# Kernel tuning notes

Hardware: AMD Instinct MI355X
Metric: run time of the kernel (lower is better)

Reference implementation:

```python
import jax, jax.numpy as jnp
import numpy as np

N_STREAMS = 4096


def setup_inputs() -> dict:
    key = jax.random.key(0)
    # Plain Gaussian (well-separated singular values; the polar factor math is
    # identical to the module's eye + 0.01*randn init, just a different point).
    H_raw = jax.random.normal(key, (N_STREAMS, N_STREAMS), dtype=jnp.float32)
    return {"H_raw": H_raw}


def reference(H_raw) -> jnp.ndarray:
    # OrthogonalMixing.forward: orthogonal polar factor of H_raw via thin SVD.
    U, s, Vh = jnp.linalg.svd(H_raw, full_matrices=False)
    return U @ Vh  # (s, s), satisfies H^T H = I
```

## Files before the change

### kernel.cpp

```cpp
#include <hip/hip_runtime.h>
#include <hip/hip_bf16.h>
#include <hip/hip_fp16.h>

#define NN 4096
#define NGROW 8
#define NPOL 2
#define NITER (NGROW + NPOL)
#define NPOW 12
#define NKT (NN / 64)
#define NTRI 136
#define PRESCALE 32.0f

using f16 = _Float16;
typedef __attribute__((ext_vector_type(4))) float f32x4;
typedef __attribute__((ext_vector_type(8))) f16 h16x8;

__device__ inline void gl_lds16(const void* g, void* l) {
  __builtin_amdgcn_global_load_lds(
      (const __attribute__((address_space(1))) unsigned int*)(unsigned long long)(uintptr_t)g,
      (__attribute__((address_space(3))) unsigned int*)(uintptr_t)l,
      16, 0, 0);
}

template <int EPI, int TRI>
__global__ __launch_bounds__(512, 2) void gemm_nt(
    const f16* __restrict__ P, const f16* __restrict__ Q,
    void* __restrict__ Out, const f16* __restrict__ aux,
    float alpha, float beta) {
  int bi, bj;
  if (TRI) {
    const int t = blockIdx.x;
    int r = (int)((sqrtf(8.0f * (float)t + 1.0f) - 1.0f) * 0.5f);
    while ((r + 1) * (r + 2) / 2 <= t) ++r;
    while (r * (r + 1) / 2 > t) --r;
    bi = r;
    bj = t - r * (r + 1) / 2;
  } else {
    bi = blockIdx.x;
    bj = blockIdx.y;
  }

  __shared__ f16 lA[2][256 * 64];
  __shared__ f16 lB[2][256 * 64];

  const int tid = threadIdx.x;
  const int lane = tid & 63;
  const int wv = tid >> 6;
  const int wr = wv >> 2;
  const int wc = wv & 3;
  const int m = lane & 15;
  const int qd = lane >> 4;
  const int srow = tid >> 3;
  const int schk = tid & 7;

  f32x4 acc[8][4] = {};
  h16x8 avA[2][2], avB[2][2];
  h16x8 bv0[4][2], bv1[4][2];

#define STAGE_A(u_, kk_, b_)                                                  \
  do {                                                                        \
    const int rr_ = (u_)*64 + srow;                                           \
    gl_lds16(P + (size_t)(bi * 256 + rr_) * NN + (kk_) + ((schk ^ (srow & 7)) * 8), \
             &lA[b_][(u_)*4096 + tid * 8]);                                   \
  } while (0)
#define STAGE_B(u_, kk_, b_)                                                  \
  do {                                                                        \
    const int rr_ = (u_)*64 + srow;                                           \
    gl_lds16(Q + (size_t)(bj * 256 + rr_) * NN + (kk_) + ((schk ^ (srow & 7)) * 8), \
             &lB[b_][(u_)*4096 + tid * 8]);                                   \
  } while (0)

#define READ_AV(dst_, b_, q_)                                                 \
  do {                                                                        \
    _Pragma("unroll") for (int rf = 0; rf < 2; ++rf)                          \
    _Pragma("unroll") for (int ks = 0; ks < 2; ++ks) {                        \
      const int ra = wr * 128 + (q_)*32 + rf * 16 + m;                        \
      const int ca = (ks * 4 + qd) ^ (ra & 7);                                \
      dst_[rf][ks] = *(const h16x8*)&lA[b_][ra * 64 + ca * 8];                \
    }                                                                         \
  } while (0)
#define READ_BV(dst_, b_)                                                     \
  do {                                                                        \
    _Pragma("unroll") for (int cf = 0; cf < 4; ++cf)                          \
    _Pragma("unroll") for (int ks = 0; ks < 2; ++ks) {                        \
      const int rb = wc * 64 + cf * 16 + m;                                   \
      const int cb = (ks * 4 + qd) ^ (rb & 7);                                \
      dst_[cf][ks] = *(const h16x8*)&lB[b_][rb * 64 + cb * 8];                \
    }                                                                         \
  } while (0)
#define MFMA_Q(q_, A_, B_)                                                    \
  do {                                                                        \
    _Pragma("unroll") for (int rf = 0; rf < 2; ++rf)                          \
    _Pragma("unroll") for (int cf = 0; cf < 4; ++cf)                          \
    _Pragma("unroll") for (int ks = 0; ks < 2; ++ks)                          \
        acc[(q_)*2 + rf][cf] = __builtin_amdgcn_mfma_f32_16x16x32_f16(        \
            A_[rf][ks], B_[cf][ks], acc[(q_)*2 + rf][cf], 0, 0, 0);           \
  } while (0)

#define BAR() __builtin_amdgcn_s_barrier()
#define VMCNT(n_) asm volatile("s_waitcnt vmcnt(" #n_ ")" ::: "memory")
#define SGB(m_, n_) __builtin_amdgcn_sched_group_barrier(m_, n_, 0)
#define SGB_RD4_ST2()                                                         \
  do { SGB(0x8,2); SGB(0x100,1); SGB(0x8,2); SGB(0x100,1); SGB(0x8,2);        \
       SGB(0x100,1); SGB(0x8,2); SGB(0x100,1); SGB(0x8,2); SGB(0x30,1);       \
       SGB(0x8,3); SGB(0x30,1); SGB(0x8,3); } while (0)
#define SGB_RD4_ST0()                                                         \
  do { SGB(0x8,3); SGB(0x100,1); SGB(0x8,3); SGB(0x100,1); SGB(0x8,3);        \
       SGB(0x100,1); SGB(0x8,3); SGB(0x100,1); SGB(0x8,4); } while (0)
#define SGB_RD12_ST2()                                                        \
  do { SGB(0x100,2); SGB(0x8,2); SGB(0x100,2); SGB(0x8,2); SGB(0x100,2);      \
       SGB(0x8,2); SGB(0x100,2); SGB(0x8,2); SGB(0x100,2); SGB(0x8,2);        \
       SGB(0x100,2); SGB(0x8,2); SGB(0x30,1); SGB(0x8,2); SGB(0x30,1);        \
       SGB(0x8,2); } while (0)
#define SGB_RD12_ST0()                                                        \
  do { SGB(0x100,2); SGB(0x8,2); SGB(0x100,2); SGB(0x8,2); SGB(0x100,2);      \
       SGB(0x8,2); SGB(0x100,2); SGB(0x8,2); SGB(0x100,2); SGB(0x8,2);        \
       SGB(0x100,2); SGB(0x8,2); SGB(0x8,4); } while (0)

#define TILE_STEADY(t_, b_, nb_, BVC_, BVN_)                                  \
  {                                                                           \
    const int k1 = ((t_) + 1) * 64, k2 = ((t_) + 2) * 64;                     \
                                                                      \
    READ_AV(avB, b_, 1);                                                      \
    STAGE_A(1, k1, nb_); STAGE_A(3, k1, nb_);                                 \
    MFMA_Q(0, avA, BVC_);                                                     \
    SGB_RD4_ST2(); BAR();                                                     \
                                                                      \
    READ_AV(avA, b_, 2);                                                      \
    STAGE_B(0, k2, b_); STAGE_B(1, k2, b_);                                   \
    MFMA_Q(1, avB, BVC_);                                                     \
    SGB_RD4_ST2(); BAR();                                                     \
                                                                      \
    READ_AV(avB, b_, 3);                                                      \
    STAGE_B(2, k2, b_); STAGE_B(3, k2, b_);                                   \
    MFMA_Q(2, avA, BVC_);                                                     \
    SGB_RD4_ST2(); VMCNT(4); BAR();                                           \
                 \
    READ_BV(BVN_, nb_);                                                       \
    READ_AV(avA, nb_, 0);                                                     \
    STAGE_A(0, k2, b_); STAGE_A(2, k2, b_);                                   \
    MFMA_Q(3, avB, BVC_);                                                     \
    SGB_RD12_ST2(); BAR();                                                    \
  }

  STAGE_B(0, 0, 0); STAGE_B(1, 0, 0); STAGE_B(2, 0, 0); STAGE_B(3, 0, 0);
  STAGE_A(0, 0, 0); STAGE_A(1, 0, 0); STAGE_A(2, 0, 0); STAGE_A(3, 0, 0);
  STAGE_B(0, 64, 1); STAGE_B(1, 64, 1); STAGE_B(2, 64, 1); STAGE_B(3, 64, 1);
  STAGE_A(0, 64, 1); STAGE_A(2, 64, 1);
  VMCNT(6);
  BAR();
  READ_BV(bv0, 0);
  READ_AV(avA, 0, 0);
  BAR();

  for (int tt = 0; tt < NKT - 2; tt += 2) {
    TILE_STEADY(tt, 0, 1, bv0, bv1);
    TILE_STEADY(tt + 1, 1, 0, bv1, bv0);
  }

  {
    READ_AV(avB, 0, 1);
    STAGE_A(1, (NKT - 1) * 64, 1); STAGE_A(3, (NKT - 1) * 64, 1);
    MFMA_Q(0, avA, bv0);
    SGB_RD4_ST2(); BAR();
    READ_AV(avA, 0, 2);
    MFMA_Q(1, avB, bv0);
    SGB_RD4_ST0(); BAR();
    READ_AV(avB, 0, 3);
    MFMA_Q(2, avA, bv0);
    SGB_RD4_ST0(); VMCNT(0); BAR();
    READ_BV(bv1, 1);
    READ_AV(avA, 1, 0);
    MFMA_Q(3, avB, bv0);
    SGB_RD12_ST0(); BAR();
  }
  {
    READ_AV(avB, 1, 1);
    MFMA_Q(0, avA, bv1);
    SGB_RD4_ST0(); BAR();
    READ_AV(avA, 1, 2);
    MFMA_Q(1, avB, bv1);
    SGB_RD4_ST0(); BAR();
    READ_AV(avB, 1, 3);
    MFMA_Q(2, avA, bv1);
    SGB_RD4_ST0(); BAR();
    MFMA_Q(3, avB, bv1);
  }

#pragma unroll
  for (int fr = 0; fr < 8; ++fr) {
#pragma unroll
    for (int fc = 0; fc < 4; ++fc) {
#pragma unroll
      for (int rg = 0; rg < 4; ++rg) {
        const int lr = wr * 128 + fr * 16 + qd * 4 + rg;
        const int lc = wc * 64 + fc * 16 + m;
        const size_t idx = (size_t)(bi * 256 + lr) * NN + bj * 256 + lc;
        float v = beta * acc[fr][fc][rg];
        if (alpha != 0.0f) v += alpha * (float)aux[idx];
        if (EPI == 0)
          ((f16*)Out)[idx] = (f16)v;
        else
          ((float*)Out)[idx] = v;
        if (TRI && bi != bj) {
          const size_t idxT = (size_t)(bj * 256 + lc) * NN + bi * 256 + lr;
          ((f16*)Out)[idxT] = (f16)v;
        }
      }
    }
  }
#undef STAGE_A
#undef STAGE_B
#undef READ_AV
#undef READ_BV
#undef MFMA_Q
#undef TILE_STEADY
#undef BAR
#undef VMCNT
#undef SGB
#undef SGB_RD4_ST2
#undef SGB_RD4_ST0
#undef SGB_RD12_ST2
#undef SGB_RD12_ST0
}

__global__ void transpose_h(const unsigned short* __restrict__ in,
                            unsigned short* __restrict__ out) {
  __shared__ unsigned short tile[64][65];
  const int tx = threadIdx.x & 63;
  const int ty = threadIdx.x >> 6;
  const int bx = blockIdx.x, by = blockIdx.y;
#pragma unroll
  for (int rr = 0; rr < 16; ++rr) {
    const int row = rr * 4 + ty;
    tile[row][tx] = in[(size_t)(by * 64 + row) * NN + bx * 64 + tx];
  }
  __syncthreads();
#pragma unroll
  for (int rr = 0; rr < 16; ++rr) {
    const int row = rr * 4 + ty;
    out[(size_t)(bx * 64 + row) * NN + by * 64 + tx] = tile[tx][row];
  }
}

__global__ __launch_bounds__(256) void powmv(const f16* __restrict__ A,
                                             const float* __restrict__ vin,
                                             const float* __restrict__ snin,
                                             float* __restrict__ vout,
                                             float* __restrict__ snout) {
  const float scale = rsqrtf(*snin);
  const int row = blockIdx.x * 4 + (threadIdx.x >> 6);
  const int lane = threadIdx.x & 63;
  const f16* arow = A + (size_t)row * NN;
  float acc = 0.0f;
#pragma unroll
  for (int p = 0; p < 8; ++p) {
    const int c = p * 512 + lane * 8;
    const h16x8 av = *(const h16x8*)(arow + c);
    const float4 w0 = *(const float4*)(vin + c);
    const float4 w1 = *(const float4*)(vin + c + 4);
    acc += (float)av[0] * w0.x + (float)av[1] * w0.y + (float)av[2] * w0.z +
           (float)av[3] * w0.w + (float)av[4] * w1.x + (float)av[5] * w1.y +
           (float)av[6] * w1.z + (float)av[7] * w1.w;
  }
  for (int off = 32; off; off >>= 1) acc += __shfl_down(acc, off, 64);
  if (lane == 0) {
    const float u = acc * scale;
    vout[row] = u;
    atomicAdd(snout, u * u);
  }
}

__global__ void init_pw(float* __restrict__ v0, float* __restrict__ slots) {
  const int t = threadIdx.x;
  if (t < 64) slots[t] = (t == 1) ? 1.0f : 0.0f;
  for (int i = t; i < NN; i += 256) {
    const unsigned h = (unsigned)i * 2654435761u;
    v0[i] = ((h >> 16) & 1) ? 0.015625f : -0.015625f;
  }
}

__global__ void reduce_sumsq(const float* __restrict__ h, float* __restrict__ slots) {
  float acc = 0.0f;
  const size_t total = (size_t)NN * NN;
  for (size_t i = (size_t)blockIdx.x * blockDim.x + threadIdx.x; i < total;
       i += (size_t)gridDim.x * blockDim.x) {
    const float v = h[i];
    acc += v * v;
  }
  for (int off = 32; off; off >>= 1) acc += __shfl_down(acc, off, 64);
  __shared__ float ws[4];
  const int lane = threadIdx.x & 63, wv = threadIdx.x >> 6;
  if (lane == 0) ws[wv] = acc;
  __syncthreads();
  if (threadIdx.x == 0) atomicAdd(&slots[0], ws[0] + ws[1] + ws[2] + ws[3]);
}

__global__ void scale_cast(const float* __restrict__ h, const float* __restrict__ slots,
                           f16* __restrict__ xb, int mode) {
  float inv = rsqrtf(slots[0]) * PRESCALE;
  if (mode) inv *= rsqrtf(1.10f * sqrtf(slots[1 + NPOW]));
  const size_t i = ((size_t)blockIdx.x * blockDim.x + threadIdx.x) * 4;
  const float4 v = *(const float4*)(h + i);
  union { f16 hh[4]; ushort4 u; } cvt;
  cvt.hh[0] = (f16)(v.x * inv);
  cvt.hh[1] = (f16)(v.y * inv);
  cvt.hh[2] = (f16)(v.z * inv);
  cvt.hh[3] = (f16)(v.w * inv);
  *(ushort4*)(xb + i) = cvt.u;
}

__global__ void rescale_f16(f16* __restrict__ a, const float* __restrict__ slots) {
  const float cA = 1.0f / (1.10f * sqrtf(slots[1 + NPOW]));
  const size_t i = ((size_t)blockIdx.x * 256 + threadIdx.x) * 8;
  h16x8 v = *(h16x8*)(a + i);
  h16x8 o;
#pragma unroll
  for (int j = 0; j < 8; ++j) o[j] = (f16)((float)v[j] * cA);
  *(h16x8*)(a + i) = o;
}

extern "C" void kernel_launch(void* const* d_in, const int* in_sizes, int n_in,
                              void* d_out, int out_size, void* d_ws, size_t ws_size,
                              hipStream_t stream) {
  (void)in_sizes; (void)n_in; (void)out_size; (void)ws_size;
  const float* H = (const float*)d_in[0];
  float* out = (float*)d_out;
  char* ws = (char*)d_ws;

  f16* P0 = (f16*)ws;
  f16* P1 = (f16*)(ws + ((size_t)32 << 20));
  f16* Ab = (f16*)(ws + ((size_t)64 << 20));
  f16* Bb = (f16*)((char*)d_out + ((size_t)32 << 20));
  float* v0 = (float*)d_out;
  float* v1 = (float*)((char*)d_out + 16384);
  float* slots = (float*)((char*)d_out + 32768);

  const dim3 gfull(16, 16), tbg(512), tb(256), gt(64, 64);

  init_pw<<<1, 256, 0, stream>>>(v0, slots);
  reduce_sumsq<<<1024, 256, 0, stream>>>(H, slots);
  scale_cast<<<(NN * (size_t)NN) / 4 / 256, 256, 0, stream>>>(H, slots, P0, 0);
  transpose_h<<<gt, tb, 0, stream>>>((const unsigned short*)P0, (unsigned short*)P1);
  gemm_nt<0, 1><<<NTRI, tbg, 0, stream>>>(P1, P1, Ab, (f16*)nullptr, 0.0f, 1.0f);
  for (int k = 0; k < NPOW; ++k) {
    const float* vi = (k & 1) ? v1 : v0;
    float* vo = (k & 1) ? v0 : v1;
    powmv<<<1024, 256, 0, stream>>>(Ab, vi, &slots[1 + k], vo, &slots[2 + k]);
  }
  rescale_f16<<<(NN * (size_t)NN) / 8 / 256, 256, 0, stream>>>(Ab, slots);
  scale_cast<<<(NN * (size_t)NN) / 4 / 256, 256, 0, stream>>>(H, slots, P0, 1);

  f16* X = P0;
  f16* Y = P1;
  const float GA = 3.4445f, GB = -4.7750f, GC = 2.0315f;
  const float PA = 1.875f, PB = -1.25f, PC = 0.375f;

  for (int it = 0; it < NITER; ++it) {
    const bool polish = it >= NGROW;
    const bool last = (it == NITER - 1);
    const float qa = polish ? PA : GA, qb = polish ? PB : GB, qc = polish ? PC : GC;

    if (it > 0) {
      transpose_h<<<gt, tb, 0, stream>>>((const unsigned short*)X, (unsigned short*)Y);
      gemm_nt<0, 1><<<NTRI, tbg, 0, stream>>>(Y, Y, Ab, (f16*)nullptr, 0.0f, 1.0f);
    }
    f16* Bdst = last ? Y : Bb;
    gemm_nt<0, 1><<<NTRI, tbg, 0, stream>>>(Ab, Ab, Bdst, Ab, qb, qc);
    if (!last) {
      gemm_nt<0, 0><<<gfull, tbg, 0, stream>>>(X, Bdst, Y, X, qa, 1.0f);
      f16* t = X; X = Y; Y = t;
    } else {
      gemm_nt<1, 0><<<gfull, tbg, 0, stream>>>(X, Bdst, out, X, qa, 1.0f);
    }
  }
}
```

Before: 4.454 ms.

## Swizzle GEMM block order across XCDs and replace sched barriers with setprio

Block indices are remapped so consecutive hardware block IDs, which are dealt round-robin across the 8 XCDs, map to contiguous tile regions per XCD. This is meant to improve L2 reuse of A/B panels. The full grid becomes 1D (256 blocks). The hand-tuned sched_group_barrier interleaving of LDS reads, stores and MFMAs is removed in favour of raising wave priority around the MFMA clusters. That leaves instruction interleaving to the compiler and may lose the memory/compute overlap the explicit schedule provided.

After: 6.731 ms. +51.1%, slower.

```diff
diff --git a/kernel.cpp b/kernel.cpp
--- a/kernel.cpp
+++ b/kernel.cpp
@@ -29,15 +29,18 @@
     float alpha, float beta) {
   int bi, bj;
   if (TRI) {
-    const int t = blockIdx.x;
+    const int t0 = blockIdx.x;
+    const int t = (t0 & 7) * 17 + (t0 >> 3);
     int r = (int)((sqrtf(8.0f * (float)t + 1.0f) - 1.0f) * 0.5f);
     while ((r + 1) * (r + 2) / 2 <= t) ++r;
     while (r * (r + 1) / 2 > t) --r;
     bi = r;
     bj = t - r * (r + 1) / 2;
   } else {
-    bi = blockIdx.x;
-    bj = blockIdx.y;
+    const int b0 = blockIdx.x;
+    const int sw = (b0 & 7) * 32 + (b0 >> 3);
+    bi = sw >> 4;
+    bj = sw & 15;
   }
 
   __shared__ f16 lA[2][256 * 64];
@@ -98,24 +101,8 @@
   } while (0)
 
 #define BAR() __builtin_amdgcn_s_barrier()
+#define PRIO(x_) __builtin_amdgcn_s_setprio(x_)
 #define VMCNT(n_) asm volatile("s_waitcnt vmcnt(" #n_ ")" ::: "memory")
-#define SGB(m_, n_) __builtin_amdgcn_sched_group_barrier(m_, n_, 0)
-#define SGB_RD4_ST2()                                                         \
-  do { SGB(0x8,2); SGB(0x100,1); SGB(0x8,2); SGB(0x100,1); SGB(0x8,2);        \
-       SGB(0x100,1); SGB(0x8,2); SGB(0x100,1); SGB(0x8,2); SGB(0x30,1);       \
-       SGB(0x8,3); SGB(0x30,1); SGB(0x8,3); } while (0)
-#define SGB_RD4_ST0()                                                         \
-  do { SGB(0x8,3); SGB(0x100,1); SGB(0x8,3); SGB(0x100,1); SGB(0x8,3);        \
-       SGB(0x100,1); SGB(0x8,3); SGB(0x100,1); SGB(0x8,4); } while (0)
-#define SGB_RD12_ST2()                                                        \
-  do { SGB(0x100,2); SGB(0x8,2); SGB(0x100,2); SGB(0x8,2); SGB(0x100,2);      \
-       SGB(0x8,2); SGB(0x100,2); SGB(0x8,2); SGB(0x100,2); SGB(0x8,2);        \
-       SGB(0x100,2); SGB(0x8,2); SGB(0x30,1); SGB(0x8,2); SGB(0x30,1);        \
-       SGB(0x8,2); } while (0)
-#define SGB_RD12_ST0()                                                        \
-  do { SGB(0x100,2); SGB(0x8,2); SGB(0x100,2); SGB(0x8,2); SGB(0x100,2);      \
-       SGB(0x8,2); SGB(0x100,2); SGB(0x8,2); SGB(0x100,2); SGB(0x8,2);        \
-       SGB(0x100,2); SGB(0x8,2); SGB(0x8,4); } while (0)
 
 #define TILE_STEADY(t_, b_, nb_, BVC_, BVN_)                                  \
   {                                                                           \
@@ -123,24 +110,24 @@
                                                                       \
     READ_AV(avB, b_, 1);                                                      \
     STAGE_A(1, k1, nb_); STAGE_A(3, k1, nb_);                                 \
-    MFMA_Q(0, avA, BVC_);                                                     \
-    SGB_RD4_ST2(); BAR();                                                     \
+    PRIO(1); MFMA_Q(0, avA, BVC_); PRIO(0);                                   \
+    BAR();                                                                    \
                                                                       \
     READ_AV(avA, b_, 2);                                                      \
     STAGE_B(0, k2, b_); STAGE_B(1, k2, b_);                                   \
-    MFMA_Q(1, avB, BVC_);                                                     \
-    SGB_RD4_ST2(); BAR();                                                     \
+    PRIO(1); MFMA_Q(1, avB, BVC_); PRIO(0);                                   \
+    BAR();                                                                    \
                                                                       \
     READ_AV(avB, b_, 3);                                                      \
     STAGE_B(2, k2, b_); STAGE_B(3, k2, b_);                                   \
-    MFMA_Q(2, avA, BVC_);                                                     \
-    SGB_RD4_ST2(); VMCNT(4); BAR();                                           \
+    PRIO(1); MFMA_Q(2, avA, BVC_); PRIO(0);                                   \
+    VMCNT(4); BAR();                                                          \
                  \
     READ_BV(BVN_, nb_);                                                       \
     READ_AV(avA, nb_, 0);                                                     \
     STAGE_A(0, k2, b_); STAGE_A(2, k2, b_);                                   \
-    MFMA_Q(3, avB, BVC_);                                                     \
-    SGB_RD12_ST2(); BAR();                                                    \
+    PRIO(1); MFMA_Q(3, avB, BVC_); PRIO(0);                                   \
+    BAR();                                                                    \
   }
 
   STAGE_B(0, 0, 0); STAGE_B(1, 0, 0); STAGE_B(2, 0, 0); STAGE_B(3, 0, 0);
@@ -161,30 +148,30 @@
   {
     READ_AV(avB, 0, 1);
     STAGE_A(1, (NKT - 1) * 64, 1); STAGE_A(3, (NKT - 1) * 64, 1);
-    MFMA_Q(0, avA, bv0);
-    SGB_RD4_ST2(); BAR();
+    PRIO(1); MFMA_Q(0, avA, bv0); PRIO(0);
+    BAR();
     READ_AV(avA, 0, 2);
-    MFMA_Q(1, avB, bv0);
-    SGB_RD4_ST0(); BAR();
+    PRIO(1); MFMA_Q(1, avB, bv0); PRIO(0);
+    BAR();
     READ_AV(avB, 0, 3);
-    MFMA_Q(2, avA, bv0);
-    SGB_RD4_ST0(); VMCNT(0); BAR();
+    PRIO(1); MFMA_Q(2, avA, bv0); PRIO(0);
+    VMCNT(0); BAR();
     READ_BV(bv1, 1);
     READ_AV(avA, 1, 0);
-    MFMA_Q(3, avB, bv0);
-    SGB_RD12_ST0(); BAR();
+    PRIO(1); MFMA_Q(3, avB, bv0); PRIO(0);
+    BAR();
   }
   {
     READ_AV(avB, 1, 1);
-    MFMA_Q(0, avA, bv1);
-    SGB_RD4_ST0(); BAR();
+    PRIO(1); MFMA_Q(0, avA, bv1); PRIO(0);
+    BAR();
     READ_AV(avA, 1, 2);
-    MFMA_Q(1, avB, bv1);
-    SGB_RD4_ST0(); BAR();
+    PRIO(1); MFMA_Q(1, avB, bv1); PRIO(0);
+    BAR();
     READ_AV(avB, 1, 3);
-    MFMA_Q(2, avA, bv1);
-    SGB_RD4_ST0(); BAR();
-    MFMA_Q(3, avB, bv1);
+    PRIO(1); MFMA_Q(2, avA, bv1); PRIO(0);
+    BAR();
+    PRIO(1); MFMA_Q(3, avB, bv1); PRIO(0);
   }
 
 #pragma unroll
@@ -216,12 +203,8 @@
 #undef MFMA_Q
 #undef TILE_STEADY
 #undef BAR
+#undef PRIO
 #undef VMCNT
-#undef SGB
-#undef SGB_RD4_ST2
-#undef SGB_RD4_ST0
-#undef SGB_RD12_ST2
-#undef SGB_RD12_ST0
 }
 
 __global__ void transpose_h(const unsigned short* __restrict__ in,
@@ -336,7 +319,7 @@
   float* v1 = (float*)((char*)d_out + 16384);
   float* slots = (float*)((char*)d_out + 32768);
 
-  const dim3 gfull(16, 16), tbg(512), tb(256), gt(64, 64);
+  const dim3 gfull(256), tbg(512), tb(256), gt(64, 64);
 
   init_pw<<<1, 256, 0, stream>>>(v0, slots);
   reduce_sumsq<<<1024, 256, 0, stream>>>(H, slots);
```
